# Performance work log

Measured on AMD Instinct MI355X. Metric: run time of the kernel, lower is better.

The kernel has to match this reference:

```python
import jax, jax.numpy as jnp
import numpy as np


def setup_inputs() -> dict:
    key = jax.random.key(0)
    ks = jax.random.split(key, 9)
    B, T, D, U = 512, 1024, 64, 128
    inp = {
        'inputs': jax.random.normal(ks[0], (B, T, D), dtype=jnp.float32),
        'W_f': jax.random.normal(ks[1], (D, U), dtype=jnp.float32) * 0.05,
        'U_f': jax.random.normal(ks[2], (U, U), dtype=jnp.float32) * 0.05,
        'b_f': jnp.zeros((U,), dtype=jnp.float32),
        'W_i': jax.random.normal(ks[3], (D, U), dtype=jnp.float32) * 0.05,
        'U_i': jax.random.normal(ks[4], (U, U), dtype=jnp.float32) * 0.05,
        'b_i': jnp.zeros((U,), dtype=jnp.float32),
        'W_c': jax.random.normal(ks[5], (D, U), dtype=jnp.float32) * 0.05,
        'U_c': jax.random.normal(ks[6], (U, U), dtype=jnp.float32) * 0.05,
        'b_c': jnp.zeros((U,), dtype=jnp.float32),
        'W_o': jax.random.normal(ks[7], (D, U), dtype=jnp.float32) * 0.05,
        'U_o': jax.random.normal(ks[8], (U, U), dtype=jnp.float32) * 0.05,
        'b_o': jnp.zeros((U,), dtype=jnp.float32),
    }
    return inp


def _lstm(inputs, W_f, U_f, b_f, W_i, U_i, b_i, W_c, U_c, b_c, W_o, U_o, b_o):
    B, T, D = inputs.shape
    U = W_f.shape[1]
    # Precompute all input-to-gate projections in one batched GEMM per gate: [B,T,U]
    xf = jnp.einsum('btd,du->btu', inputs, W_f) + b_f
    xi = jnp.einsum('btd,du->btu', inputs, W_i) + b_i
    xc = jnp.einsum('btd,du->btu', inputs, W_c) + b_c
    xo = jnp.einsum('btd,du->btu', inputs, W_o) + b_o
    # time-major stacked gate inputs: [T, B, 4, U]
    xg = jnp.stack([xf, xi, xc, xo], axis=2).transpose(1, 0, 2, 3)
    # concatenated recurrent weights: [U, 4U]
    U_all = jnp.concatenate([U_f, U_i, U_c, U_o], axis=1)

    def step(carry, x_t):
        h, c = carry
        # x_t: [B, 4, U]
        rec = (h @ U_all).reshape(B, 4, U)
        g = x_t + rec
        f = jax.nn.sigmoid(g[:, 0])
        i = jax.nn.sigmoid(g[:, 1])
        c_tilde = jnp.tanh(g[:, 2])
        o = jax.nn.sigmoid(g[:, 3])
        c_new = f * c + i * c_tilde
        h_new = o * jnp.tanh(c_new)
        return (h_new, c_new), None

    h0 = jnp.zeros((B, U), dtype=inputs.dtype)
    c0 = jnp.zeros((B, U), dtype=inputs.dtype)
    (h, c), _ = jax.lax.scan(step, (h0, c0), xg)
    return h


def reference(inputs, W_f, U_f, b_f, W_i, U_i, b_i, W_c, U_c, b_c, W_o, U_o, b_o):
    return _lstm(inputs, W_f, U_f, b_f, W_i, U_i, b_i, W_c, U_c, b_c, W_o, U_o, b_o)
```

## Files before the change

### kernel.cpp

```cpp
#include <hip/hip_runtime.h>
#include <stdint.h>


typedef __attribute__((ext_vector_type(8))) short short8;
typedef __attribute__((ext_vector_type(4))) float floatx4;
typedef __attribute__((ext_vector_type(4))) int   intx4;
typedef __attribute__((ext_vector_type(8))) int   intx8;

#define B_SZ   512
#define T_SZ   1024
#define D_SZ   64
#define U_SZ   128
#define ROWS   2
#define NBLK   (B_SZ / ROWS)
#define NTHR   512
#define A1STRB 160
#define A2STR  72
#define GXSTR  524

__device__ __forceinline__ short f2bf(float f) {
    uint32_t u = __builtin_bit_cast(uint32_t, f);
    uint32_t r = (u + 0x7fffu + ((u >> 16) & 1u)) >> 16;
    return (short)r;
}
__device__ __forceinline__ float fsig(float x) {
    return __builtin_amdgcn_rcpf(1.0f + __builtin_amdgcn_exp2f(-1.4426950408889634f * x));
}
__device__ __forceinline__ float ftanh(float x) {
    return 1.0f - 2.0f * __builtin_amdgcn_rcpf(1.0f + __builtin_amdgcn_exp2f(2.8853900817779268f * x));
}
__device__ __forceinline__ void sync_lds() {
    asm volatile("s_waitcnt lgkmcnt(0)\n\ts_barrier" ::: "memory");
}

__global__ __launch_bounds__(NTHR, 2) void lstm_persistent(
    const float* __restrict__ xin,
    const float* __restrict__ Wf, const float* __restrict__ Uf, const float* __restrict__ bfp,
    const float* __restrict__ Wi, const float* __restrict__ Ui, const float* __restrict__ bip,
    const float* __restrict__ Wc, const float* __restrict__ Uc, const float* __restrict__ bcp,
    const float* __restrict__ Wo, const float* __restrict__ Uo, const float* __restrict__ bop,
    float* __restrict__ out)
{
    __shared__ float Gx[16 * GXSTR];
    __shared__ __align__(16) char A1[2][2 * A1STRB];
    __shared__ short A2[16 * A2STR];

    const int tid  = threadIdx.x;
    const int wave = tid >> 6;
    const int lane = tid & 63;
    const int quad = lane >> 4;
    const int nlo  = lane & 15;
    const int blk  = blockIdx.x;

    const int  u      = 16 * wave + nlo;
    const int  prow   = quad >> 1;
    const bool writer = (quad & 1) == 0;

    const float* Wg[4] = {Wf, Wi, Wc, Wo};
    const float* Ug[4] = {Uf, Ui, Uc, Uo};

    intx8 bU8[4];
#pragma unroll
    for (int g = 0; g < 4; ++g) {
#pragma unroll
        for (int d = 0; d < 8; ++d) {
            const int k0 = quad * 32 + d * 4;
            float w0 = Ug[g][(k0 + 0) * U_SZ + u];
            float w1 = Ug[g][(k0 + 1) * U_SZ + u];
            float w2 = Ug[g][(k0 + 2) * U_SZ + u];
            float w3 = Ug[g][(k0 + 3) * U_SZ + u];
            int pk = __builtin_amdgcn_cvt_pk_fp8_f32(w0, w1, 0, 0);
            pk     = __builtin_amdgcn_cvt_pk_fp8_f32(w2, w3, pk, 1);
            bU8[g][d] = pk;
        }
    }
    short8 bW[4][2];
#pragma unroll
    for (int g = 0; g < 4; ++g)
#pragma unroll
        for (int kt = 0; kt < 2; ++kt)
#pragma unroll
            for (int j = 0; j < 8; ++j) {
                int k = kt * 32 + quad * 8 + j;
                bW[g][kt][j] = f2bf(Wg[g][k * U_SZ + u]);
            }
    const float bias4[4] = {bfp[u], bip[u], bcp[u], bop[u]};
    float c_st = 0.0f;

    const int xrow = tid >> 8;
    const int xj   = (tid >> 5) & 7;
    const int xd   = (tid & 31) << 1;
    const float* xb = xin + ((size_t)(blk * ROWS + xrow) * T_SZ) * D_SZ + xd;

    for (int i = tid; i < 2 * 2 * A1STRB; i += NTHR) ((char*)A1)[i] = 0;
    {
        float2 v = *(const float2*)(xb + (size_t)xj * D_SZ);
        short2 p; p.x = f2bf(v.x); p.y = f2bf(v.y);
        *(short2*)&A2[(2 * xj + xrow) * A2STR + xd] = p;
    }
    __syncthreads();
    {
        const short* a2p = &A2[nlo * A2STR + quad * 8];
        short8 s0 = *(const short8*)a2p, s1 = *(const short8*)(a2p + 32);
        floatx4 q[4];
#pragma unroll
        for (int g = 0; g < 4; ++g) {
            q[g] = (floatx4){0.f, 0.f, 0.f, 0.f};
            q[g] = __builtin_amdgcn_mfma_f32_16x16x32_bf16(s0, bW[g][0], q[g], 0, 0, 0);
            q[g] = __builtin_amdgcn_mfma_f32_16x16x32_bf16(s1, bW[g][1], q[g], 0, 0, 0);
        }
#pragma unroll
        for (int r = 0; r < 4; ++r) {
            floatx4 wv = {q[0][r] + bias4[0], q[1][r] + bias4[1],
                          q[2][r] + bias4[2], q[3][r] + bias4[3]};
            *(floatx4*)&Gx[(quad * 4 + r) * GXSTR + 4 * u] = wv;
        }
    }
    float2 xr = *(const float2*)(xb + (size_t)(8 + xj) * D_SZ);
    __syncthreads();

    for (int g = 0; g < 128; ++g) {
#pragma unroll
        for (int j = 0; j < 8; ++j) {
            const int s = g * 8 + j;

            if (j == 0 && g < 127) {
                short2 p; p.x = f2bf(xr.x); p.y = f2bf(xr.y);
                *(short2*)&A2[(2 * xj + xrow) * A2STR + xd] = p;
            }
            if (j == 2 && g < 126) {
                xr = *(const float2*)(xb + (size_t)(8 * (g + 2) + xj) * D_SZ);
            }

            const char* ap = &A1[j & 1][(nlo & 1) * A1STRB + quad * 32];
            intx4 alo = *(const intx4*)(ap);
            intx4 ahi = *(const intx4*)(ap + 16);
            intx8 a8 = {alo.x, alo.y, alo.z, alo.w, ahi.x, ahi.y, ahi.z, ahi.w};

            floatx4 acc[4];
#pragma unroll
            for (int gt = 0; gt < 4; ++gt) {
                floatx4 z = (floatx4){0.f, 0.f, 0.f, 0.f};
                acc[gt] = __builtin_amdgcn_mfma_scale_f32_16x16x128_f8f6f4(
                    a8, bU8[gt], z, 0, 0,
                    0, 0x7f7f7f7f,
                    0, 0x7f7f7f7f);
            }

            floatx4 gx = *(const floatx4*)&Gx[(2 * j + prow) * GXSTR + 4 * u];

            float gv0 = (prow ? acc[0][1] : acc[0][0]) + gx[0];
            float gv1 = (prow ? acc[1][1] : acc[1][0]) + gx[1];
            float gv2 = (prow ? acc[2][1] : acc[2][0]) + gx[2];
            float gv3 = (prow ? acc[3][1] : acc[3][0]) + gx[3];
            float f  = fsig(gv0);
            float ii = fsig(gv1);
            float ct = ftanh(gv2);
            float oo = fsig(gv3);
            c_st = f * c_st + ii * ct;
            float h = oo * ftanh(c_st);

            float hnb = __shfl_xor(h, 1);
            if (s == T_SZ - 1) {
                if (writer) out[(size_t)(blk * ROWS + prow) * U_SZ + u] = h;
            } else if (writer && (nlo & 1) == 0) {
                int pk = __builtin_amdgcn_cvt_pk_fp8_f32(h, hnb, 0, 0);
                *(short*)&A1[(j & 1) ^ 1][prow * A1STRB + u] = (short)(pk & 0xffff);
            }

            if (j == 7 && g < 127) {
                const short* a2p = &A2[nlo * A2STR + quad * 8];
                short8 s0 = *(const short8*)a2p, s1 = *(const short8*)(a2p + 32);
                floatx4 q[4];
#pragma unroll
                for (int gt = 0; gt < 4; ++gt) {
                    q[gt] = (floatx4){0.f, 0.f, 0.f, 0.f};
                    q[gt] = __builtin_amdgcn_mfma_f32_16x16x32_bf16(s0, bW[gt][0], q[gt], 0, 0, 0);
                    q[gt] = __builtin_amdgcn_mfma_f32_16x16x32_bf16(s1, bW[gt][1], q[gt], 0, 0, 0);
                }
                sync_lds();
#pragma unroll
                for (int r = 0; r < 4; ++r) {
                    floatx4 wv = {q[0][r] + bias4[0], q[1][r] + bias4[1],
                                  q[2][r] + bias4[2], q[3][r] + bias4[3]};
                    *(floatx4*)&Gx[(quad * 4 + r) * GXSTR + 4 * u] = wv;
                }
            }

            sync_lds();
        }
    }
}

extern "C" void kernel_launch(void* const* d_in, const int* in_sizes, int n_in,
                              void* d_out, int out_size, void* d_ws, size_t ws_size,
                              hipStream_t stream) {
    (void)in_sizes; (void)n_in; (void)d_ws; (void)ws_size; (void)out_size;
    const float* xin = (const float*)d_in[0];
    const float* Wf  = (const float*)d_in[1];
    const float* Uf  = (const float*)d_in[2];
    const float* bf  = (const float*)d_in[3];
    const float* Wi  = (const float*)d_in[4];
    const float* Ui  = (const float*)d_in[5];
    const float* bi  = (const float*)d_in[6];
    const float* Wc  = (const float*)d_in[7];
    const float* Uc  = (const float*)d_in[8];
    const float* bc  = (const float*)d_in[9];
    const float* Wo  = (const float*)d_in[10];
    const float* Uo  = (const float*)d_in[11];
    const float* bo  = (const float*)d_in[12];
    float* out = (float*)d_out;

    hipLaunchKernelGGL(lstm_persistent, dim3(NBLK), dim3(NTHR), 0, stream,
                       xin, Wf, Uf, bf, Wi, Ui, bi, Wc, Uc, bc, Wo, Uo, bo, out);
}
```

Baseline: 581.9 us.

## Halve block to 4 waves, each wave computing two 16-unit column tiles

```diff
diff --git a/kernel.cpp b/kernel.cpp
--- a/kernel.cpp
+++ b/kernel.cpp
@@ -3,6 +3,7 @@
 
 
 typedef __attribute__((ext_vector_type(8))) short short8;
+typedef __attribute__((ext_vector_type(4))) short short4v;
 typedef __attribute__((ext_vector_type(4))) float floatx4;
 typedef __attribute__((ext_vector_type(4))) int   intx4;
 typedef __attribute__((ext_vector_type(8))) int   intx8;
@@ -13,7 +14,7 @@
 #define U_SZ   128
 #define ROWS   2
 #define NBLK   (B_SZ / ROWS)
-#define NTHR   512
+#define NTHR   256
 #define A1STRB 160
 #define A2STR  72
 #define GXSTR  524
@@ -33,7 +34,7 @@
     asm volatile("s_waitcnt lgkmcnt(0)\n\ts_barrier" ::: "memory");
 }
 
-__global__ __launch_bounds__(NTHR, 2) void lstm_persistent(
+__global__ __launch_bounds__(NTHR, 1) void lstm_persistent(
     const float* __restrict__ xin,
     const float* __restrict__ Wf, const float* __restrict__ Uf, const float* __restrict__ bfp,
     const float* __restrict__ Wi, const float* __restrict__ Ui, const float* __restrict__ bip,
@@ -52,71 +53,86 @@
     const int nlo  = lane & 15;
     const int blk  = blockIdx.x;
 
-    const int  u      = 16 * wave + nlo;
-    const int  prow   = quad >> 1;
-    const bool writer = (quad & 1) == 0;
+    const int ti_s = quad & 1;
+    const int prow = quad >> 1;
+    const int u_s  = 32 * wave + 16 * ti_s + nlo;
 
     const float* Wg[4] = {Wf, Wi, Wc, Wo};
     const float* Ug[4] = {Uf, Ui, Uc, Uo};
 
-    intx8 bU8[4];
-#pragma unroll
-    for (int g = 0; g < 4; ++g) {
-#pragma unroll
-        for (int d = 0; d < 8; ++d) {
-            const int k0 = quad * 32 + d * 4;
-            float w0 = Ug[g][(k0 + 0) * U_SZ + u];
-            float w1 = Ug[g][(k0 + 1) * U_SZ + u];
-            float w2 = Ug[g][(k0 + 2) * U_SZ + u];
-            float w3 = Ug[g][(k0 + 3) * U_SZ + u];
-            int pk = __builtin_amdgcn_cvt_pk_fp8_f32(w0, w1, 0, 0);
-            pk     = __builtin_amdgcn_cvt_pk_fp8_f32(w2, w3, pk, 1);
-            bU8[g][d] = pk;
-        }
-    }
-    short8 bW[4][2];
+    intx8 bU8[4][2];
 #pragma unroll
     for (int g = 0; g < 4; ++g)
 #pragma unroll
-        for (int kt = 0; kt < 2; ++kt)
-#pragma unroll
-            for (int j = 0; j < 8; ++j) {
-                int k = kt * 32 + quad * 8 + j;
-                bW[g][kt][j] = f2bf(Wg[g][k * U_SZ + u]);
-            }
-    const float bias4[4] = {bfp[u], bip[u], bcp[u], bop[u]};
+        for (int ti = 0; ti < 2; ++ti) {
+            const int uc = 32 * wave + 16 * ti + nlo;
+#pragma unroll
+            for (int d = 0; d < 8; ++d) {
+                const int k0 = quad * 32 + d * 4;
+                int pk = __builtin_amdgcn_cvt_pk_fp8_f32(
+                    Ug[g][(k0 + 0) * U_SZ + uc], Ug[g][(k0 + 1) * U_SZ + uc], 0, 0);
+                pk = __builtin_amdgcn_cvt_pk_fp8_f32(
+                    Ug[g][(k0 + 2) * U_SZ + uc], Ug[g][(k0 + 3) * U_SZ + uc], pk, 1);
+                bU8[g][ti][d] = pk;
+            }
+        }
+    short8 bW[4][2][2];
+#pragma unroll
+    for (int g = 0; g < 4; ++g)
+#pragma unroll
+        for (int ti = 0; ti < 2; ++ti) {
+            const int uc = 32 * wave + 16 * ti + nlo;
+#pragma unroll
+            for (int kt = 0; kt < 2; ++kt)
+#pragma unroll
+                for (int j = 0; j < 8; ++j) {
+                    int k = kt * 32 + quad * 8 + j;
+                    bW[g][ti][kt][j] = f2bf(Wg[g][k * U_SZ + uc]);
+                }
+        }
+    float biasT[2][4];
+#pragma unroll
+    for (int ti = 0; ti < 2; ++ti) {
+        const int uc = 32 * wave + 16 * ti + nlo;
+        biasT[ti][0] = bfp[uc]; biasT[ti][1] = bip[uc];
+        biasT[ti][2] = bcp[uc]; biasT[ti][3] = bop[uc];
+    }
     float c_st = 0.0f;
 
-    const int xrow = tid >> 8;
-    const int xj   = (tid >> 5) & 7;
-    const int xd   = (tid & 31) << 1;
+    const int xrow = tid >> 7;
+    const int xj   = (tid >> 4) & 7;
+    const int xd   = (tid & 15) << 2;
     const float* xb = xin + ((size_t)(blk * ROWS + xrow) * T_SZ) * D_SZ + xd;
 
     for (int i = tid; i < 2 * 2 * A1STRB; i += NTHR) ((char*)A1)[i] = 0;
     {
-        float2 v = *(const float2*)(xb + (size_t)xj * D_SZ);
-        short2 p; p.x = f2bf(v.x); p.y = f2bf(v.y);
-        *(short2*)&A2[(2 * xj + xrow) * A2STR + xd] = p;
+        float4 v = *(const float4*)(xb + (size_t)xj * D_SZ);
+        short4v p = {f2bf(v.x), f2bf(v.y), f2bf(v.z), f2bf(v.w)};
+        *(short4v*)&A2[(2 * xj + xrow) * A2STR + xd] = p;
     }
     __syncthreads();
     {
         const short* a2p = &A2[nlo * A2STR + quad * 8];
         short8 s0 = *(const short8*)a2p, s1 = *(const short8*)(a2p + 32);
-        floatx4 q[4];
-#pragma unroll
-        for (int g = 0; g < 4; ++g) {
-            q[g] = (floatx4){0.f, 0.f, 0.f, 0.f};
-            q[g] = __builtin_amdgcn_mfma_f32_16x16x32_bf16(s0, bW[g][0], q[g], 0, 0, 0);
-            q[g] = __builtin_amdgcn_mfma_f32_16x16x32_bf16(s1, bW[g][1], q[g], 0, 0, 0);
-        }
-#pragma unroll
-        for (int r = 0; r < 4; ++r) {
-            floatx4 wv = {q[0][r] + bias4[0], q[1][r] + bias4[1],
-                          q[2][r] + bias4[2], q[3][r] + bias4[3]};
-            *(floatx4*)&Gx[(quad * 4 + r) * GXSTR + 4 * u] = wv;
-        }
-    }
-    float2 xr = *(const float2*)(xb + (size_t)(8 + xj) * D_SZ);
+#pragma unroll
+        for (int ti = 0; ti < 2; ++ti) {
+            floatx4 q[4];
+#pragma unroll
+            for (int g = 0; g < 4; ++g) {
+                q[g] = (floatx4){0.f, 0.f, 0.f, 0.f};
+                q[g] = __builtin_amdgcn_mfma_f32_16x16x32_bf16(s0, bW[g][ti][0], q[g], 0, 0, 0);
+                q[g] = __builtin_amdgcn_mfma_f32_16x16x32_bf16(s1, bW[g][ti][1], q[g], 0, 0, 0);
+            }
+            const int uc = 32 * wave + 16 * ti + nlo;
+#pragma unroll
+            for (int r = 0; r < 4; ++r) {
+                floatx4 wv = {q[0][r] + biasT[ti][0], q[1][r] + biasT[ti][1],
+                              q[2][r] + biasT[ti][2], q[3][r] + biasT[ti][3]};
+                *(floatx4*)&Gx[(quad * 4 + r) * GXSTR + 4 * uc] = wv;
+            }
+        }
+    }
+    float4 xr = *(const float4*)(xb + (size_t)(8 + xj) * D_SZ);
     __syncthreads();
 
     for (int g = 0; g < 128; ++g) {
@@ -125,34 +141,40 @@
             const int s = g * 8 + j;
 
             if (j == 0 && g < 127) {
-                short2 p; p.x = f2bf(xr.x); p.y = f2bf(xr.y);
-                *(short2*)&A2[(2 * xj + xrow) * A2STR + xd] = p;
+                short4v p = {f2bf(xr.x), f2bf(xr.y), f2bf(xr.z), f2bf(xr.w)};
+                *(short4v*)&A2[(2 * xj + xrow) * A2STR + xd] = p;
             }
             if (j == 2 && g < 126) {
-                xr = *(const float2*)(xb + (size_t)(8 * (g + 2) + xj) * D_SZ);
+                xr = *(const float4*)(xb + (size_t)(8 * (g + 2) + xj) * D_SZ);
             }
 
             const char* ap = &A1[j & 1][(nlo & 1) * A1STRB + quad * 32];
             intx4 alo = *(const intx4*)(ap);
             intx4 ahi = *(const intx4*)(ap + 16);
+            floatx4 gx = *(const floatx4*)&Gx[(2 * j + prow) * GXSTR + 4 * u_s];
             intx8 a8 = {alo.x, alo.y, alo.z, alo.w, ahi.x, ahi.y, ahi.z, ahi.w};
 
-            floatx4 acc[4];
-#pragma unroll
-            for (int gt = 0; gt < 4; ++gt) {
-                floatx4 z = (floatx4){0.f, 0.f, 0.f, 0.f};
-                acc[gt] = __builtin_amdgcn_mfma_scale_f32_16x16x128_f8f6f4(
-                    a8, bU8[gt], z, 0, 0,
-                    0, 0x7f7f7f7f,
-                    0, 0x7f7f7f7f);
-            }
-
-            floatx4 gx = *(const floatx4*)&Gx[(2 * j + prow) * GXSTR + 4 * u];
-
-            float gv0 = (prow ? acc[0][1] : acc[0][0]) + gx[0];
-            float gv1 = (prow ? acc[1][1] : acc[1][0]) + gx[1];
-            float gv2 = (prow ? acc[2][1] : acc[2][0]) + gx[2];
-            float gv3 = (prow ? acc[3][1] : acc[3][0]) + gx[3];
+            floatx4 acc[4][2];
+#pragma unroll
+            for (int gt = 0; gt < 4; ++gt)
+#pragma unroll
+                for (int ti = 0; ti < 2; ++ti) {
+                    floatx4 z = (floatx4){0.f, 0.f, 0.f, 0.f};
+                    acc[gt][ti] = __builtin_amdgcn_mfma_scale_f32_16x16x128_f8f6f4(
+                        a8, bU8[gt][ti], z, 0, 0,
+                        0, 0x7f7f7f7f,
+                        0, 0x7f7f7f7f);
+                }
+
+            float gv0 = (ti_s ? (prow ? acc[0][1][1] : acc[0][1][0])
+                              : (prow ? acc[0][0][1] : acc[0][0][0])) + gx[0];
+            float gv1 = (ti_s ? (prow ? acc[1][1][1] : acc[1][1][0])
+                              : (prow ? acc[1][0][1] : acc[1][0][0])) + gx[1];
+            float gv2 = (ti_s ? (prow ? acc[2][1][1] : acc[2][1][0])
+                              : (prow ? acc[2][0][1] : acc[2][0][0])) + gx[2];
+            float gv3 = (ti_s ? (prow ? acc[3][1][1] : acc[3][1][0])
+                              : (prow ? acc[3][0][1] : acc[3][0][0])) + gx[3];
+
             float f  = fsig(gv0);
             float ii = fsig(gv1);
             float ct = ftanh(gv2);
@@ -162,28 +184,34 @@
 
             float hnb = __shfl_xor(h, 1);
             if (s == T_SZ - 1) {
-                if (writer) out[(size_t)(blk * ROWS + prow) * U_SZ + u] = h;
-            } else if (writer && (nlo & 1) == 0) {
+                out[(size_t)(blk * ROWS + prow) * U_SZ + u_s] = h;
+            } else if ((nlo & 1) == 0) {
                 int pk = __builtin_amdgcn_cvt_pk_fp8_f32(h, hnb, 0, 0);
-                *(short*)&A1[(j & 1) ^ 1][prow * A1STRB + u] = (short)(pk & 0xffff);
+                *(short*)&A1[(j & 1) ^ 1][prow * A1STRB + u_s] = (short)(pk & 0xffff);
             }
 
             if (j == 7 && g < 127) {
                 const short* a2p = &A2[nlo * A2STR + quad * 8];
                 short8 s0 = *(const short8*)a2p, s1 = *(const short8*)(a2p + 32);
-                floatx4 q[4];
-#pragma unroll
-                for (int gt = 0; gt < 4; ++gt) {
-                    q[gt] = (floatx4){0.f, 0.f, 0.f, 0.f};
-                    q[gt] = __builtin_amdgcn_mfma_f32_16x16x32_bf16(s0, bW[gt][0], q[gt], 0, 0, 0);
-                    q[gt] = __builtin_amdgcn_mfma_f32_16x16x32_bf16(s1, bW[gt][1], q[gt], 0, 0, 0);
-                }
+                floatx4 q[4][2];
+#pragma unroll
+                for (int ti = 0; ti < 2; ++ti)
+#pragma unroll
+                    for (int gt = 0; gt < 4; ++gt) {
+                        q[gt][ti] = (floatx4){0.f, 0.f, 0.f, 0.f};
+                        q[gt][ti] = __builtin_amdgcn_mfma_f32_16x16x32_bf16(s0, bW[gt][ti][0], q[gt][ti], 0, 0, 0);
+                        q[gt][ti] = __builtin_amdgcn_mfma_f32_16x16x32_bf16(s1, bW[gt][ti][1], q[gt][ti], 0, 0, 0);
+                    }
                 sync_lds();
 #pragma unroll
-                for (int r = 0; r < 4; ++r) {
-                    floatx4 wv = {q[0][r] + bias4[0], q[1][r] + bias4[1],
-                                  q[2][r] + bias4[2], q[3][r] + bias4[3]};
-                    *(floatx4*)&Gx[(quad * 4 + r) * GXSTR + 4 * u] = wv;
+                for (int ti = 0; ti < 2; ++ti) {
+                    const int uc = 32 * wave + 16 * ti + nlo;
+#pragma unroll
+                    for (int r = 0; r < 4; ++r) {
+                        floatx4 wv = {q[0][ti][r] + biasT[ti][0], q[1][ti][r] + biasT[ti][1],
+                                      q[2][ti][r] + biasT[ti][2], q[3][ti][r] + biasT[ti][3]};
+                        *(floatx4*)&Gx[(quad * 4 + r) * GXSTR + 4 * uc] = wv;
+                    }
                 }
             }
 
```

New measurement: 597.0 us. 2.6% more time.
